# Optimization experiments

Hardware: AMD Instinct MI355X
Metric: run time of the kernel (lower is better)

The kernel has to match this reference:

```python
import jax, jax.numpy as jnp
import numpy as np

NUM_HEAD = 8   # in_channels // 64 for in_channels=512
DIM = 8        # per-head dim (== num_head in this module)
H_CH = NUM_HEAD * DIM  # 64
SCALE = DIM ** (-0.5)


def _conv(x, w, b, padding):
    # x: [N,C,H,W], w: [O,I,kh,kw]
    out = jax.lax.conv_general_dilated(
        x, w, window_strides=(1, 1), padding=padding,
        dimension_numbers=("NCHW", "OIHW", "NCHW"))
    return out + b[None, :, None, None]


def setup_inputs() -> dict:
    key = jax.random.key(0)
    ks = jax.random.split(key, 4)
    N, C, H, W = 4, 512, 48, 48
    x = jax.random.normal(ks[0], (N, C, H, W), dtype=jnp.float32)
    qkv_w = jax.random.normal(ks[1], (3 * H_CH, C, 1, 1), dtype=jnp.float32) * 0.05
    qkv_b = jnp.zeros((3 * H_CH,), dtype=jnp.float32)
    pos_w = jax.random.normal(ks[2], (H_CH, H_CH, 3, 3), dtype=jnp.float32) * 0.05
    pos_b = jnp.zeros((H_CH,), dtype=jnp.float32)
    res_w = jax.random.normal(ks[3], (C, H_CH, 1, 1), dtype=jnp.float32) * 0.05
    res_b = jnp.zeros((C,), dtype=jnp.float32)
    return {"x": x, "qkv_w": qkv_w, "qkv_b": qkv_b,
            "pos_w": pos_w, "pos_b": pos_b,
            "res_w": res_w, "res_b": res_b}


def reference(x, qkv_w, qkv_b, pos_w, pos_b, res_w, res_b):
    N, C, H, W = x.shape
    L = H * W
    # 1x1 conv QKV projection -> [N, 3h, H, W]
    qkv = _conv(x, qkv_w, qkv_b, "VALID")
    # [N, num_head, 3*dim, L]
    qkv = qkv.reshape(N, NUM_HEAD, 3 * DIM, L)
    q, k, v = qkv[:, :, :DIM], qkv[:, :, DIM:2 * DIM], qkv[:, :, 2 * DIM:]
    # attn = q^T @ k * scale : [N, nh, L, L], softmax over keys (last dim)
    attn = jnp.einsum("nhdq,nhdk->nhqk", q, k) * SCALE
    attn = jax.nn.softmax(attn, axis=-1)
    # out = v @ attn^T : [N, nh, dim, L]
    out = jnp.einsum("nhdk,nhqk->nhdq", v, attn)
    out = out.reshape(N, H_CH, H, W)
    # positional branch: 3x3 conv on v
    pos = _conv(v.reshape(N, H_CH, H, W), pos_w, pos_b, "SAME")
    out = out + pos
    # resume 1x1 conv -> [N, out_channels, H, W]
    return _conv(out, res_w, res_b, "VALID")
```

## Files before the change

### kernel.cpp

```cpp
#include <hip/hip_runtime.h>

#define L_ATT 2304
#define QSCALE_LOG2E 0.5100695712f

using bh8 = __attribute__((ext_vector_type(8))) short;
using f4  = __attribute__((ext_vector_type(4))) float;

#if __has_builtin(__builtin_amdgcn_exp2f)
#define EXP2(x) __builtin_amdgcn_exp2f(x)
#else
#define EXP2(x) exp2f(x)
#endif

__device__ inline short f2b(float f) {
    union { float f; unsigned u; } c; c.f = f;
    unsigned r = (c.u + 0x7FFFu + ((c.u >> 16) & 1u)) >> 16;
    return (short)r;
}
__device__ inline float b2f(short s) {
    union { unsigned u; float f; } c;
    c.u = ((unsigned)(unsigned short)s) << 16;
    return c.f;
}
__device__ inline int packhi(float lo, float hi) {
    return (int)__builtin_amdgcn_perm(__float_as_uint(hi), __float_as_uint(lo), 0x07060302u);
}

__global__ __launch_bounds__(256) void prep_kernel(
    const float* __restrict__ x, const float* __restrict__ qkv_w,
    const float* __restrict__ res_w, const float* __restrict__ pos_w,
    short* __restrict__ xt, short* __restrict__ wqb,
    short* __restrict__ reswb, short* __restrict__ wqp)
{
    __shared__ float s[64][68];
    const int g = blockIdx.x;
    if (g < 272) {
        int j = g * 256 + threadIdx.x;
        if (j < 24576) {
            float4 v = ((const float4*)qkv_w)[j];
            short4 o = { f2b(v.x), f2b(v.y), f2b(v.z), f2b(v.w) };
            *(short4*)(wqb + (size_t)j * 4) = o;
        } else if (j < 32768) {
            int idx = j - 24576;
            float4 v = ((const float4*)res_w)[idx];
            short4 o = { f2b(v.x), f2b(v.y), f2b(v.z), f2b(v.w) };
            *(short4*)(reswb + (size_t)idx * 4) = o;
        } else {
            int e = j - 32768;
            wqp[e] = f2b(pos_w[(size_t)(e & 4095) * 9 + (e >> 12)]);
        }
        return;
    }
    const int gg = g - 272;
    const int l0 = (gg % 36) * 64, k0 = ((gg / 36) & 7) * 64, n = gg / 288;
    const int tr = threadIdx.x >> 4, tc4 = (threadIdx.x & 15) * 4;
    const float* xp = x + ((size_t)n * 512 + k0) * L_ATT + l0;
#pragma unroll
    for (int r = 0; r < 4; ++r)
        *(float4*)&s[tr + r * 16][tc4] =
            *(const float4*)(xp + (size_t)(tr + r * 16) * L_ATT + tc4);
    __syncthreads();
    short* op = xt + ((size_t)n * L_ATT + l0) * 512 + k0;
#pragma unroll
    for (int r = 0; r < 4; ++r) {
        int l = tr + r * 16;
        short4 o = { f2b(s[tc4 + 0][l]), f2b(s[tc4 + 1][l]),
                     f2b(s[tc4 + 2][l]), f2b(s[tc4 + 3][l]) };
        *(short4*)(op + (size_t)l * 512 + tc4) = o;
    }
}

__global__ __launch_bounds__(256) void qkv_kernel(
    const short* __restrict__ xt, const short* __restrict__ wqb,
    const float* __restrict__ qkv_b, short* __restrict__ qt8,
    short* __restrict__ kt8, short* __restrict__ vt, short* __restrict__ vle)
{
    const int g = blockIdx.x;
    const int xcd = g & 7, rr = g >> 3;
    const int y = rr % 3, grp = rr / 3;
    const int code = grp * 8 + xcd;
    const int l0 = (code % 72) * 32, oc0 = y * 64, n = code / 72;

    const int lane = threadIdx.x & 63, wave = threadIdx.x >> 6;
    const int col = lane & 15, quad = lane >> 4;
    const int ocb = oc0 + wave * 16;

    f4 acc[2];
    acc[0] = (f4){0.f, 0.f, 0.f, 0.f};
    acc[1] = (f4){0.f, 0.f, 0.f, 0.f};

    const short* arow = wqb + (size_t)(ocb + col) * 512 + quad * 8;
    const short* brow = xt + ((size_t)n * L_ATT + l0 + col) * 512 + quad * 8;

#pragma unroll 4
    for (int k0 = 0; k0 < 512; k0 += 32) {
        bh8 af = *(const bh8*)(arow + k0);
        bh8 b0 = *(const bh8*)(brow + k0);
        bh8 b1 = *(const bh8*)(brow + (size_t)16 * 512 + k0);
        acc[0] = __builtin_amdgcn_mfma_f32_16x16x32_bf16(af, b0, acc[0], 0, 0, 0);
        acc[1] = __builtin_amdgcn_mfma_f32_16x16x32_bf16(af, b1, acc[1], 0, 0, 0);
    }

    const int obase = ocb + quad * 4;
    const int h = obase / 24;
    const int r0 = obase - h * 24;
    const int slice = n * 8 + h;

#pragma unroll
    for (int nt = 0; nt < 2; ++nt) {
        int l = l0 + nt * 16 + col;
        float v[4];
#pragma unroll
        for (int reg = 0; reg < 4; ++reg) v[reg] = acc[nt][reg] + qkv_b[obase + reg];
        if (r0 < 8) {
            short4 o = { f2b(v[0] * QSCALE_LOG2E), f2b(v[1] * QSCALE_LOG2E),
                         f2b(v[2] * QSCALE_LOG2E), f2b(v[3] * QSCALE_LOG2E) };
            *(short4*)(qt8 + ((size_t)slice * L_ATT + l) * 8 + r0) = o;
        } else if (r0 < 16) {
            short4 o = { f2b(v[0]), f2b(v[1]), f2b(v[2]), f2b(v[3]) };
            *(short4*)(kt8 + ((size_t)slice * L_ATT + l) * 8 + (r0 - 8)) = o;
        } else {
            short4 o = { f2b(v[0]), f2b(v[1]), f2b(v[2]), f2b(v[3]) };
            int d0 = r0 - 16;
#pragma unroll
            for (int reg = 0; reg < 4; ++reg)
                vt[((size_t)slice * 8 + d0 + reg) * L_ATT + l] = ((short*)&o)[reg];
            *(short4*)(vle + ((size_t)n * L_ATT + l) * 64 + h * 8 + d0) = o;
        }
    }
}

__global__ __launch_bounds__(256) void attnpos_kernel(
    const short* __restrict__ qt8, const short* __restrict__ kt8,
    const short* __restrict__ vt, const short* __restrict__ vle,
    const short* __restrict__ wqp, const float* __restrict__ pbias,
    float* __restrict__ pnum, float* __restrict__ pls, short* __restrict__ pcv)
{
    __shared__ short smem[2064];
    const int g = blockIdx.x;
    const int tid = threadIdx.x;
    const int lane = tid & 63, wave = tid >> 6;
    const int col = lane & 15, quad = lane >> 4;

    if (g < 1152) {
        const int h = g & 7, r = g >> 3;
        const int n = r / 36;
        const int rem = r - n * 36;
        const int qt = rem >> 1, half = rem & 1;
        const int q0 = qt * 128;
        const int kbase = half * 1152;
        const int slice = n * 8 + h;

        const short* qs  = qt8 + (size_t)slice * L_ATT * 8;
        const short* ks8 = kt8 + (size_t)slice * L_ATT * 8;
        const short* vb  = vt  + (size_t)slice * 8 * L_ATT;

        if (tid < 16) smem[2048 + tid] = (tid < 8) ? (short)0x3F80 : (short)0;

        bh8 zero8 = {0, 0, 0, 0, 0, 0, 0, 0};
        bh8 qf[2];
#pragma unroll
        for (int f = 0; f < 2; ++f) {
            qf[f] = zero8;
            if (quad == 0)
                qf[f] = *(const bh8*)(qs + (size_t)(q0 + wave * 32 + f * 16 + col) * 8);
        }

        const int kxor = (quad == 0) ? 512 : 0;
        int kidx[4];
#pragma unroll
        for (int nt = 0; nt < 4; ++nt)
            kidx[nt] = (quad == 0) ? (nt * 16 + col) * 8 : 2056;
        const int vxor = (col < 8) ? 512 : 0;
        int vidx[2];
#pragma unroll
        for (int ks = 0; ks < 2; ++ks)
            vidx[ks] = (col < 8)
                     ? 1024 + col * 64 + ((ks * 32 + quad * 8 + col * 8) & 63)
                     : ((col == 8) ? 2048 : 2056);

        const int ksl = ((lane >> 5) & 1) * 32 + ((lane >> 2) & 1) * 16
                      + ((lane >> 3) & 3) * 4 + (lane & 3);
        const int vd = lane >> 3, vkc = (lane & 7) * 8;
        const int vsl = 1024 + vd * 64 + ((vkc + vd * 8) & 63);

        if (wave == 0)
            *(uint4*)&smem[ksl * 8] = *(const uint4*)(ks8 + (size_t)(kbase + lane) * 8);
        else if (wave == 1)
            *(uint4*)&smem[vsl] = *(const uint4*)(vb + (size_t)vd * L_ATT + kbase + vkc);
        __syncthreads();

        f4 oacc[2];
        oacc[0] = (f4){0.f, 0.f, 0.f, 0.f};
        oacc[1] = (f4){0.f, 0.f, 0.f, 0.f};

        int sofs = 512;
        for (int t = 0; t < 18; ++t) {
            uint4 dk, dv;
            if (wave == 0)
                dk = *(const uint4*)(ks8 + (size_t)(kbase + (t + 1) * 64 + lane) * 8);
            else if (wave == 1)
                dv = *(const uint4*)(vb + (size_t)vd * L_ATT + kbase + (t + 1) * 64 + vkc);

            bh8 kf[4], vf[2];
#pragma unroll
            for (int nt = 0; nt < 4; ++nt) kf[nt] = *(const bh8*)&smem[kidx[nt]];
#pragma unroll
            for (int ks = 0; ks < 2; ++ks) vf[ks] = *(const bh8*)&smem[vidx[ks]];

#pragma unroll
            for (int f = 0; f < 2; ++f) {
                f4 s[4];
#pragma unroll
                for (int nt = 0; nt < 4; ++nt) {
                    f4 z = (f4){0.f, 0.f, 0.f, 0.f};
                    s[nt] = __builtin_amdgcn_mfma_f32_16x16x32_bf16(kf[nt], qf[f], z, 0, 0, 0);
                }
                float e[4][4];
#pragma unroll
                for (int nt = 0; nt < 4; ++nt)
#pragma unroll
                    for (int reg = 0; reg < 4; ++reg)
                        e[nt][reg] = EXP2(s[nt][reg]);
#pragma unroll
                for (int ks = 0; ks < 2; ++ks) {
                    union { int i[4]; bh8 v; } pu;
                    pu.i[0] = packhi(e[2 * ks][0],     e[2 * ks][1]);
                    pu.i[1] = packhi(e[2 * ks][2],     e[2 * ks][3]);
                    pu.i[2] = packhi(e[2 * ks + 1][0], e[2 * ks + 1][1]);
                    pu.i[3] = packhi(e[2 * ks + 1][2], e[2 * ks + 1][3]);
                    oacc[f] = __builtin_amdgcn_mfma_f32_16x16x32_bf16(vf[ks], pu.v, oacc[f], 0, 0, 0);
                }
            }

            if (wave == 0)      *(uint4*)&smem[sofs + ksl * 8] = dk;
            else if (wave == 1) *(uint4*)&smem[sofs + vsl] = dv;

#pragma unroll
            for (int nt = 0; nt < 4; ++nt) kidx[nt] ^= kxor;
            vidx[0] ^= vxor; vidx[1] ^= vxor;
            sofs ^= 512;
            __syncthreads();
        }

        const size_t prow = (size_t)(slice * 2 + half) * L_ATT;
#pragma unroll
        for (int f = 0; f < 2; ++f) {
            int qg = q0 + wave * 32 + f * 16 + col;
            if (quad < 2) {
                float4 o = { oacc[f][0], oacc[f][1], oacc[f][2], oacc[f][3] };
                *(float4*)(pnum + (prow + qg) * 8 + quad * 4) = o;
            } else if (quad == 2) {
                pls[prow + qg] = oacc[f][0];
            }
        }
        return;
    }

    const int gf = g - 1152;
    const int l0 = (gf % 144) * 16, n = gf / 144;
    const int t = wave;

    const int la = l0 + col;
    const int ya = la / 48, xa = la - ya * 48;

    f4 acc = (f4){0.f, 0.f, 0.f, 0.f};
    const short* vbase = vle + (size_t)n * L_ATT * 64;

#pragma unroll
    for (int q = 0; q < 9; ++q) {
        const int dy = q / 3 - 1, dx = q - (q / 3) * 3 - 1;
        const bool valid = ((unsigned)(ya + dy) < 48u) && ((unsigned)(xa + dx) < 48u);
        const short* ap = vbase + (size_t)(la + dy * 48 + dx) * 64 + quad * 8;
#pragma unroll
        for (int ks = 0; ks < 2; ++ks) {
            bh8 af = {0, 0, 0, 0, 0, 0, 0, 0};
            if (valid) af = *(const bh8*)(ap + ks * 32);
            bh8 bf = *(const bh8*)(wqp + ((size_t)q * 64 + t * 16 + col) * 64
                                   + ks * 32 + quad * 8);
            acc = __builtin_amdgcn_mfma_f32_16x16x32_bf16(af, bf, acc, 0, 0, 0);
        }
    }

    short* op = pcv + (size_t)n * L_ATT * 64;
    const int oc = t * 16 + col;
    const float bb = pbias[oc];
#pragma unroll
    for (int reg = 0; reg < 4; ++reg) {
        int l = l0 + quad * 4 + reg;
        op[(size_t)l * 64 + oc] = f2b(acc[reg] + bb);
    }
}

__global__ __launch_bounds__(256) void res_kernel(
    const float* __restrict__ pnum, const float* __restrict__ pls,
    const short* __restrict__ pcv, const short* __restrict__ reswb,
    const float* __restrict__ res_b, float* __restrict__ out)
{
    const int g = blockIdx.x;
    const int xcd = g & 7, rr = g >> 3;
    const int y = rr & 7, grp = rr >> 3;
    const int code = grp * 8 + xcd;
    const int l0 = (code % 36) * 64, oc0 = y * 64, n = code / 36;

    const int lane = threadIdx.x & 63, wave = threadIdx.x >> 6;
    const int col = lane & 15, quad = lane >> 4;
    const int ocb = oc0 + wave * 16;

    f4 acc[4];
#pragma unroll
    for (int nt = 0; nt < 4; ++nt) acc[nt] = (f4){0.f, 0.f, 0.f, 0.f};

#pragma unroll
    for (int ks = 0; ks < 2; ++ks) {
        bh8 af = *(const bh8*)(reswb + (size_t)(ocb + col) * 64 + ks * 32 + quad * 8);
        const int h = ks * 4 + quad;
        const size_t p0 = (size_t)((n * 8 + h) * 2) * L_ATT;
        const size_t p1 = p0 + L_ATT;
#pragma unroll
        for (int nt = 0; nt < 4; ++nt) {
            const int l = l0 + nt * 16 + col;
            float4 a0 = *(const float4*)(pnum + (p0 + l) * 8);
            float4 a1 = *(const float4*)(pnum + (p0 + l) * 8 + 4);
            float4 b0 = *(const float4*)(pnum + (p1 + l) * 8);
            float4 b1 = *(const float4*)(pnum + (p1 + l) * 8 + 4);
            float inv = 1.0f / (pls[p0 + l] + pls[p1 + l]);
            bh8 pv = *(const bh8*)(pcv + ((size_t)n * L_ATT + l) * 64
                                   + ks * 32 + quad * 8);
            union { int i[4]; bh8 v; } pu;
            pu.i[0] = packhi((a0.x + b0.x) * inv + b2f(pv[0]),
                             (a0.y + b0.y) * inv + b2f(pv[1]));
            pu.i[1] = packhi((a0.z + b0.z) * inv + b2f(pv[2]),
                             (a0.w + b0.w) * inv + b2f(pv[3]));
            pu.i[2] = packhi((a1.x + b1.x) * inv + b2f(pv[4]),
                             (a1.y + b1.y) * inv + b2f(pv[5]));
            pu.i[3] = packhi((a1.z + b1.z) * inv + b2f(pv[6]),
                             (a1.w + b1.w) * inv + b2f(pv[7]));
            acc[nt] = __builtin_amdgcn_mfma_f32_16x16x32_bf16(af, pu.v, acc[nt], 0, 0, 0);
        }
    }

#pragma unroll
    for (int nt = 0; nt < 4; ++nt) {
        int l = l0 + nt * 16 + col;
#pragma unroll
        for (int reg = 0; reg < 4; ++reg) {
            int oc = ocb + quad * 4 + reg;
            out[((size_t)n * 512 + oc) * L_ATT + l] = acc[nt][reg] + res_b[oc];
        }
    }
}

extern "C" void kernel_launch(void* const* d_in, const int* in_sizes, int n_in,
                              void* d_out, int out_size, void* d_ws, size_t ws_size,
                              hipStream_t stream)
{
    const float* x      = (const float*)d_in[0];
    const float* qkv_w  = (const float*)d_in[1];
    const float* qkv_b  = (const float*)d_in[2];
    const float* pos_w  = (const float*)d_in[3];
    const float* pos_b  = (const float*)d_in[4];
    const float* res_w  = (const float*)d_in[5];
    const float* res_b  = (const float*)d_in[6];
    float* out = (float*)d_out;

    char* ws = (char*)d_ws;
    short* xt    = (short*)(ws);
    float* pnum  = (float*)(ws);
    float* pls   = (float*)(ws + 4718592);
    short* qt8   = (short*)(ws + 9437184);
    short* kt8   = (short*)(ws + 10616832);
    short* vt    = (short*)(ws + 11796480);
    short* pcv   = (short*)(ws + 12976128);
    short* wqb   = (short*)(ws + 14155776);
    short* reswb = (short*)(ws + 14352384);
    short* vle   = (short*)(ws + 14417920);
    short* wqp   = (short*)(ws + 15597568);

    prep_kernel<<<1424, 256, 0, stream>>>(x, qkv_w, res_w, pos_w, xt, wqb, reswb, wqp);
    qkv_kernel<<<864, 256, 0, stream>>>(xt, wqb, qkv_b, qt8, kt8, vt, vle);
    attnpos_kernel<<<1728, 256, 0, stream>>>(qt8, kt8, vt, vle, wqp, pos_b, pnum, pls, pcv);
    res_kernel<<<1152, 256, 0, stream>>>(pnum, pls, pcv, reswb, res_b, out);
}
```

Before: 153.4 us.

## Drop key-range split in attention; normalize in-kernel and write final attention output

The attention blocks no longer split the 2304 keys into two halves. Each block now walks all 36 key tiles, normalizes by the row sum (taken with a lane shuffle), and writes a normalized [n, L, 64] fp32 output. The residual kernel then reads one contiguous 8-float chunk instead of two partial numerators plus two partial sums. This removes partial-result traffic and the combine math. In exchange, attention blocks drop from 1152 to 576, so less parallelism may hide latency on the chip and each block runs a longer serial loop.

```diff
diff --git a/kernel.cpp b/kernel.cpp
--- a/kernel.cpp
+++ b/kernel.cpp
@@ -134,7 +134,7 @@
     const short* __restrict__ qt8, const short* __restrict__ kt8,
     const short* __restrict__ vt, const short* __restrict__ vle,
     const short* __restrict__ wqp, const float* __restrict__ pbias,
-    float* __restrict__ pnum, float* __restrict__ pls, short* __restrict__ pcv)
+    float* __restrict__ att, short* __restrict__ pcv)
 {
     __shared__ short smem[2064];
     const int g = blockIdx.x;
@@ -142,13 +142,10 @@
     const int lane = tid & 63, wave = tid >> 6;
     const int col = lane & 15, quad = lane >> 4;
 
-    if (g < 1152) {
+    if (g < 576) {
         const int h = g & 7, r = g >> 3;
-        const int n = r / 36;
-        const int rem = r - n * 36;
-        const int qt = rem >> 1, half = rem & 1;
+        const int n = r / 18, qt = r % 18;
         const int q0 = qt * 128;
-        const int kbase = half * 1152;
         const int slice = n * 8 + h;
 
         const short* qs  = qt8 + (size_t)slice * L_ATT * 8;
@@ -185,9 +182,9 @@
         const int vsl = 1024 + vd * 64 + ((vkc + vd * 8) & 63);
 
         if (wave == 0)
-            *(uint4*)&smem[ksl * 8] = *(const uint4*)(ks8 + (size_t)(kbase + lane) * 8);
+            *(uint4*)&smem[ksl * 8] = *(const uint4*)(ks8 + (size_t)lane * 8);
         else if (wave == 1)
-            *(uint4*)&smem[vsl] = *(const uint4*)(vb + (size_t)vd * L_ATT + kbase + vkc);
+            *(uint4*)&smem[vsl] = *(const uint4*)(vb + (size_t)vd * L_ATT + vkc);
         __syncthreads();
 
         f4 oacc[2];
@@ -195,12 +192,12 @@
         oacc[1] = (f4){0.f, 0.f, 0.f, 0.f};
 
         int sofs = 512;
-        for (int t = 0; t < 18; ++t) {
+        for (int t = 0; t < 36; ++t) {
             uint4 dk, dv;
             if (wave == 0)
-                dk = *(const uint4*)(ks8 + (size_t)(kbase + (t + 1) * 64 + lane) * 8);
+                dk = *(const uint4*)(ks8 + (size_t)((t + 1) * 64 + lane) * 8);
             else if (wave == 1)
-                dv = *(const uint4*)(vb + (size_t)vd * L_ATT + kbase + (t + 1) * 64 + vkc);
+                dv = *(const uint4*)(vb + (size_t)vd * L_ATT + (t + 1) * 64 + vkc);
 
             bh8 kf[4], vf[2];
 #pragma unroll
@@ -243,21 +240,21 @@
             __syncthreads();
         }
 
-        const size_t prow = (size_t)(slice * 2 + half) * L_ATT;
 #pragma unroll
         for (int f = 0; f < 2; ++f) {
-            int qg = q0 + wave * 32 + f * 16 + col;
+            float ls  = __shfl(oacc[f][0], 32 + col);
+            float inv = 1.0f / ls;
             if (quad < 2) {
-                float4 o = { oacc[f][0], oacc[f][1], oacc[f][2], oacc[f][3] };
-                *(float4*)(pnum + (prow + qg) * 8 + quad * 4) = o;
-            } else if (quad == 2) {
-                pls[prow + qg] = oacc[f][0];
+                int q = q0 + wave * 32 + f * 16 + col;
+                float4 o = { oacc[f][0] * inv, oacc[f][1] * inv,
+                             oacc[f][2] * inv, oacc[f][3] * inv };
+                *(float4*)(att + ((size_t)n * L_ATT + q) * 64 + h * 8 + quad * 4) = o;
             }
         }
         return;
     }
 
-    const int gf = g - 1152;
+    const int gf = g - 576;
     const int l0 = (gf % 144) * 16, n = gf / 144;
     const int t = wave;
 
@@ -293,9 +290,9 @@
 }
 
 __global__ __launch_bounds__(256) void res_kernel(
-    const float* __restrict__ pnum, const float* __restrict__ pls,
-    const short* __restrict__ pcv, const short* __restrict__ reswb,
-    const float* __restrict__ res_b, float* __restrict__ out)
+    const float* __restrict__ att, const short* __restrict__ pcv,
+    const short* __restrict__ reswb, const float* __restrict__ res_b,
+    float* __restrict__ out)
 {
     const int g = blockIdx.x;
     const int xcd = g & 7, rr = g >> 3;
@@ -314,28 +311,19 @@
 #pragma unroll
     for (int ks = 0; ks < 2; ++ks) {
         bh8 af = *(const bh8*)(reswb + (size_t)(ocb + col) * 64 + ks * 32 + quad * 8);
-        const int h = ks * 4 + quad;
-        const size_t p0 = (size_t)((n * 8 + h) * 2) * L_ATT;
-        const size_t p1 = p0 + L_ATT;
+        const int ch = ks * 32 + quad * 8;
 #pragma unroll
         for (int nt = 0; nt < 4; ++nt) {
             const int l = l0 + nt * 16 + col;
-            float4 a0 = *(const float4*)(pnum + (p0 + l) * 8);
-            float4 a1 = *(const float4*)(pnum + (p0 + l) * 8 + 4);
-            float4 b0 = *(const float4*)(pnum + (p1 + l) * 8);
-            float4 b1 = *(const float4*)(pnum + (p1 + l) * 8 + 4);
-            float inv = 1.0f / (pls[p0 + l] + pls[p1 + l]);
-            bh8 pv = *(const bh8*)(pcv + ((size_t)n * L_ATT + l) * 64
-                                   + ks * 32 + quad * 8);
+            const float* ab = att + ((size_t)n * L_ATT + l) * 64 + ch;
+            float4 a0 = *(const float4*)ab;
+            float4 a1 = *(const float4*)(ab + 4);
+            bh8 pv = *(const bh8*)(pcv + ((size_t)n * L_ATT + l) * 64 + ch);
             union { int i[4]; bh8 v; } pu;
-            pu.i[0] = packhi((a0.x + b0.x) * inv + b2f(pv[0]),
-                             (a0.y + b0.y) * inv + b2f(pv[1]));
-            pu.i[1] = packhi((a0.z + b0.z) * inv + b2f(pv[2]),
-                             (a0.w + b0.w) * inv + b2f(pv[3]));
-            pu.i[2] = packhi((a1.x + b1.x) * inv + b2f(pv[4]),
-                             (a1.y + b1.y) * inv + b2f(pv[5]));
-            pu.i[3] = packhi((a1.z + b1.z) * inv + b2f(pv[6]),
-                             (a1.w + b1.w) * inv + b2f(pv[7]));
+            pu.i[0] = packhi(a0.x + b2f(pv[0]), a0.y + b2f(pv[1]));
+            pu.i[1] = packhi(a0.z + b2f(pv[2]), a0.w + b2f(pv[3]));
+            pu.i[2] = packhi(a1.x + b2f(pv[4]), a1.y + b2f(pv[5]));
+            pu.i[3] = packhi(a1.z + b2f(pv[6]), a1.w + b2f(pv[7]));
             acc[nt] = __builtin_amdgcn_mfma_f32_16x16x32_bf16(af, pu.v, acc[nt], 0, 0, 0);
         }
     }
@@ -366,8 +354,7 @@
 
     char* ws = (char*)d_ws;
     short* xt    = (short*)(ws);
-    float* pnum  = (float*)(ws);
-    float* pls   = (float*)(ws + 4718592);
+    float* att   = (float*)(ws);
     short* qt8   = (short*)(ws + 9437184);
     short* kt8   = (short*)(ws + 10616832);
     short* vt    = (short*)(ws + 11796480);
@@ -379,6 +366,6 @@
 
     prep_kernel<<<1424, 256, 0, stream>>>(x, qkv_w, res_w, pos_w, xt, wqb, reswb, wqp);
     qkv_kernel<<<864, 256, 0, stream>>>(xt, wqb, qkv_b, qt8, kt8, vt, vle);
-    attnpos_kernel<<<1728, 256, 0, stream>>>(qt8, kt8, vt, vle, wqp, pos_b, pnum, pls, pcv);
-    res_kernel<<<1152, 256, 0, stream>>>(pnum, pls, pcv, reswb, res_b, out);
-}
+    attnpos_kernel<<<1152, 256, 0, stream>>>(qt8, kt8, vt, vle, wqp, pos_b, att, pcv);
+    res_kernel<<<1152, 256, 0, stream>>>(att, pcv, reswb, res_b, out);
+}
```

Measured after the change: 163.3 us. 1.06x slower.
